# Kernel tuning notes

Hardware: AMD Instinct MI355X
Metric: run time of the kernel (lower is better)

The kernel has to match this reference:

```python
import jax, jax.numpy as jnp
import numpy as np
from jax import lax

H = 1024
L = 9


def setup_inputs() -> dict:
    key = jax.random.key(0)
    ks = jax.random.split(key, 10)
    B, T = 64, 512
    hidden_states = jax.random.normal(ks[0], (B, T, H), dtype=jnp.float32)
    attention_mask = jnp.ones((B, T), dtype=jnp.int32)
    labels = jax.random.randint(ks[1], (B, T), 0, L).astype(jnp.int64)
    W1 = 0.02 * jax.random.normal(ks[2], (H, H // 2), dtype=jnp.float32)
    b1 = jnp.zeros((H // 2,), dtype=jnp.float32)
    W2 = 0.02 * jax.random.normal(ks[3], (H // 2, L), dtype=jnp.float32)
    b2 = jnp.zeros((L,), dtype=jnp.float32)
    start_transitions = 0.1 * jax.random.normal(ks[4], (L,), dtype=jnp.float32)
    end_transitions = 0.1 * jax.random.normal(ks[5], (L,), dtype=jnp.float32)
    transitions = 0.1 * jax.random.normal(ks[6], (L, L), dtype=jnp.float32)
    return {"hidden_states": hidden_states, "attention_mask": attention_mask,
            "labels": labels, "W1": W1, "b1": b1, "W2": W2, "b2": b2,
            "start_transitions": start_transitions,
            "end_transitions": end_transitions, "transitions": transitions}


def crf_nll(logits, tags, mask, start_t, end_t, trans):
    """torchcrf negative mean log-likelihood. logits [B,T,L], tags [B,T], mask [B,T] bool."""
    emis = jnp.swapaxes(logits, 0, 1)          # [T,B,L]
    tg = jnp.swapaxes(tags, 0, 1)              # [T,B]
    m = jnp.swapaxes(mask, 0, 1).astype(logits.dtype)  # [T,B]

    # --- numerator: score of the gold path ---
    e0 = jnp.take_along_axis(emis[0], tg[0][:, None], axis=1)[:, 0]
    score0 = start_t[tg[0]] + e0

    def num_step(carry, inp):
        score, prev = carry
        e, t, mi = inp
        step = trans[prev, t] + jnp.take_along_axis(e, t[:, None], axis=1)[:, 0]
        score = score + step * mi
        prev = jnp.where(mi > 0, t, prev)
        return (score, prev), None

    (num, last_tag), _ = lax.scan(num_step, (score0, tg[0]), (emis[1:], tg[1:], m[1:]))
    num = num + end_t[last_tag]

    # --- denominator: forward algorithm (log partition) ---
    alpha0 = start_t[None, :] + emis[0]        # [B,L]

    def den_step(alpha, inp):
        e, mi = inp
        nxt = jax.nn.logsumexp(alpha[:, :, None] + trans[None, :, :] + e[:, None, :], axis=1)
        return jnp.where(mi[:, None] > 0, nxt, alpha), None

    alpha, _ = lax.scan(den_step, alpha0, (emis[1:], m[1:]))
    den = jax.nn.logsumexp(alpha + end_t[None, :], axis=1)

    return -jnp.mean(num - den)


def reference(hidden_states, attention_mask, labels, W1, b1, W2, b2,
              start_transitions, end_transitions, transitions):
    # dropout is identity in eval mode
    x = jax.nn.relu(hidden_states @ W1 + b1)
    logits = x @ W2 + b2                        # [B,T,L]

    valid = labels != -100
    crf_labels = jnp.where(valid, labels, 0)
    mask = (attention_mask.astype(bool)) & valid
    mask = mask.at[:, 0].set(True)              # first timestep always on

    loss = crf_nll(logits, crf_labels, mask,
                   start_transitions, end_transitions, transitions)
    return logits, loss
```

## Files before the change

kernel.cpp:

```cpp
#include <hip/hip_runtime.h>
#include <hip/hip_bf16.h>

#define B_  64
#define T_  512
#define H_  1024
#define HC  512
#define L9  9

typedef short short8 __attribute__((ext_vector_type(8)));
typedef float f32x16 __attribute__((ext_vector_type(16)));

__device__ __forceinline__ unsigned short f2bf(float x) {
  unsigned u = __float_as_uint(x);
  u += 0x7FFFu + ((u >> 16) & 1u);
  return (unsigned short)(u >> 16);
}
__device__ __forceinline__ float bf2f(unsigned short h) {
  return __uint_as_float(((unsigned)h) << 16);
}

__device__ __forceinline__ void gload_lds16(const void* g, void* l) {
  __builtin_amdgcn_global_load_lds((const __attribute__((address_space(1))) unsigned*)g,
                                   (__attribute__((address_space(3))) unsigned*)l, 16, 0, 0);
}

__global__ void conv_w1(const float* __restrict__ w1, unsigned short* __restrict__ w1b) {
  int idx = blockIdx.x * 256 + threadIdx.x;
  int n = idx & 511, kq = idx >> 9;
  float x0 = w1[(kq * 4 + 0) * HC + n];
  float x1 = w1[(kq * 4 + 1) * HC + n];
  float x2 = w1[(kq * 4 + 2) * HC + n];
  float x3 = w1[(kq * 4 + 3) * HC + n];
  uint2 d;
  d.x = (unsigned)f2bf(x0) | ((unsigned)f2bf(x1) << 16);
  d.y = (unsigned)f2bf(x2) | ((unsigned)f2bf(x3) << 16);
  *(uint2*)(w1b + n * 1024 + kq * 4) = d;
}

__global__ __launch_bounds__(256, 2) void gemm1(
    const float* __restrict__ hs, const unsigned short* __restrict__ w1b,
    const float* __restrict__ b1, const float* __restrict__ w2,
    const float* __restrict__ b2, float* __restrict__ logits, float* __restrict__ wsE)
{
  __shared__ __align__(16) unsigned char smem[80128];
  unsigned short* ldsA = (unsigned short*)smem;
  unsigned short* ldsB = (unsigned short*)(smem + 8192);

  const int tid  = threadIdx.x;
  const int lane = tid & 63;
  const int w    = tid >> 6;
  const int row0 = blockIdx.x * 64;

  f32x16 acc[2][4];
  #pragma unroll
  for (int m = 0; m < 2; ++m)
    #pragma unroll
    for (int n = 0; n < 4; ++n)
      #pragma unroll
      for (int e = 0; e < 16; ++e) acc[m][n][e] = 0.f;

  const int arow = tid >> 2;
  const int aj4  = tid & 3;
  const float* aSrc = hs + (size_t)(row0 + arow) * H_ + aj4 * 16;
  unsigned short* aDst0 = ldsA + arow * 64 + (((aj4 * 2 + 0) ^ (arow & 7)) * 8);
  unsigned short* aDst1 = ldsA + arow * 64 + (((aj4 * 2 + 1) ^ (arow & 7)) * 8);

  const int bn   = lane >> 3;
  const int bjsw = ((lane & 7) ^ bn) * 8;

  for (int kt = 0; kt < 16; ++kt) {
    const int k0 = kt * 64;
    float4 v0 = *(const float4*)(aSrc + k0);
    float4 v1 = *(const float4*)(aSrc + k0 + 4);
    float4 v2 = *(const float4*)(aSrc + k0 + 8);
    float4 v3 = *(const float4*)(aSrc + k0 + 12);
    uint4 p0, p1;
    p0.x = (unsigned)f2bf(v0.x) | ((unsigned)f2bf(v0.y) << 16);
    p0.y = (unsigned)f2bf(v0.z) | ((unsigned)f2bf(v0.w) << 16);
    p0.z = (unsigned)f2bf(v1.x) | ((unsigned)f2bf(v1.y) << 16);
    p0.w = (unsigned)f2bf(v1.z) | ((unsigned)f2bf(v1.w) << 16);
    p1.x = (unsigned)f2bf(v2.x) | ((unsigned)f2bf(v2.y) << 16);
    p1.y = (unsigned)f2bf(v2.z) | ((unsigned)f2bf(v2.w) << 16);
    p1.z = (unsigned)f2bf(v3.x) | ((unsigned)f2bf(v3.y) << 16);
    p1.w = (unsigned)f2bf(v3.z) | ((unsigned)f2bf(v3.w) << 16);
    *(uint4*)aDst0 = p0;
    *(uint4*)aDst1 = p1;
    #pragma unroll
    for (int i = 0; i < 16; ++i) {
      int cc = w * 16 + i;
      gload_lds16(w1b + (size_t)(cc * 8 + bn) * 1024 + k0 + bjsw,
                  (unsigned char*)ldsB + cc * 1024);
    }
    __syncthreads();
    #pragma unroll
    for (int ks = 0; ks < 4; ++ks) {
      const int blk = (((ks * 2 + (lane >> 5)) ^ (lane & 7)) * 8);
      short8 aF[2], bF[4];
      #pragma unroll
      for (int m = 0; m < 2; ++m)
        aF[m] = *(const short8*)(ldsA + (m * 32 + (lane & 31)) * 64 + blk);
      #pragma unroll
      for (int n = 0; n < 4; ++n)
        bF[n] = *(const short8*)(ldsB + (w * 128 + n * 32 + (lane & 31)) * 64 + blk);
      #pragma unroll
      for (int m = 0; m < 2; ++m)
        #pragma unroll
        for (int n = 0; n < 4; ++n)
          acc[m][n] = __builtin_amdgcn_mfma_f32_32x32x16_bf16(aF[m], bF[n], acc[m][n], 0, 0, 0);
    }
    __syncthreads();
  }

  float b1v[4];
  #pragma unroll
  for (int n = 0; n < 4; ++n) b1v[n] = b1[w * 128 + n * 32 + (lane & 31)];

  #pragma unroll
  for (int m = 0; m < 2; ++m)
    #pragma unroll
    for (int n = 0; n < 4; ++n) {
      int col = w * 128 + n * 32 + (lane & 31);
      int csw = col & 7;
      unsigned char* cbase = smem + col * 128 + (lane >> 5) * 8;
      #pragma unroll
      for (int q = 0; q < 4; ++q) {
        unsigned short h0 = f2bf(fmaxf(acc[m][n][q * 4 + 0] + b1v[n], 0.f));
        unsigned short h1 = f2bf(fmaxf(acc[m][n][q * 4 + 1] + b1v[n], 0.f));
        unsigned short h2 = f2bf(fmaxf(acc[m][n][q * 4 + 2] + b1v[n], 0.f));
        unsigned short h3 = f2bf(fmaxf(acc[m][n][q * 4 + 3] + b1v[n], 0.f));
        uint2 d;
        d.x = (unsigned)h0 | ((unsigned)h1 << 16);
        d.y = (unsigned)h2 | ((unsigned)h3 << 16);
        *(uint2*)(cbase + (((4 * m + q) ^ csw) * 16)) = d;
      }
    }

  unsigned short* ldsW2 = (unsigned short*)(smem + 65536);
  float* sAcc = (float*)(smem + 77824);
  {
    int c0 = tid * 2;
    #pragma unroll
    for (int cc = c0; cc < c0 + 2; ++cc)
      #pragma unroll
      for (int l = 0; l < 9; ++l) ldsW2[cc * 12 + l] = f2bf(w2[cc * 9 + l]);
    for (int i = tid; i < 576; i += 256) sAcc[i] = 0.f;
  }
  __syncthreads();

  {
    int r = tid & 63, ch = tid >> 6;
    int rblk = r >> 3, rlow = r & 7;
    float s[9];
    #pragma unroll
    for (int l = 0; l < 9; ++l) s[l] = 0.f;
    for (int c = ch * 128; c < ch * 128 + 128; ++c) {
      float xv = bf2f(*(const unsigned short*)(smem + c * 128 + ((rblk ^ (c & 7)) * 16) + rlow * 2));
      uint2 wa = *(const uint2*)(ldsW2 + c * 12);
      uint2 wb = *(const uint2*)(ldsW2 + c * 12 + 4);
      unsigned wcv = *(const unsigned*)(ldsW2 + c * 12 + 8);
      s[0] = fmaf(xv, __uint_as_float(wa.x << 16), s[0]);
      s[1] = fmaf(xv, __uint_as_float(wa.x & 0xFFFF0000u), s[1]);
      s[2] = fmaf(xv, __uint_as_float(wa.y << 16), s[2]);
      s[3] = fmaf(xv, __uint_as_float(wa.y & 0xFFFF0000u), s[3]);
      s[4] = fmaf(xv, __uint_as_float(wb.x << 16), s[4]);
      s[5] = fmaf(xv, __uint_as_float(wb.x & 0xFFFF0000u), s[5]);
      s[6] = fmaf(xv, __uint_as_float(wb.y << 16), s[6]);
      s[7] = fmaf(xv, __uint_as_float(wb.y & 0xFFFF0000u), s[7]);
      s[8] = fmaf(xv, __uint_as_float(wcv << 16), s[8]);
    }
    #pragma unroll
    for (int l = 0; l < 9; ++l) atomicAdd(&sAcc[r * 9 + l], s[l]);
  }
  __syncthreads();

  {
    int bb = row0 >> 9, t0g = row0 & 511;
    for (int v = tid; v < 576; v += 256) {
      int r = v / 9, l = v - r * 9;
      float val = sAcc[v] + b2[l];
      logits[(size_t)(row0 + r) * 9 + l] = val;
      wsE[(size_t)((t0g + r) * 9 + l) * 64 + bb] = __expf(val);
    }
  }
}

#define NCH 64
#define CHL 8
__global__ __launch_bounds__(64, 1) void crf_chunks(
    const float* __restrict__ wsE, const int* __restrict__ labels,
    const int* __restrict__ amask, const float* __restrict__ logits,
    const float* __restrict__ trans, float* __restrict__ wsG)
{
  __shared__ float sT[81];
  int b = threadIdx.x;
  for (int i = b; i < 81; i += 64) sT[i] = trans[i];
  __syncthreads();
  int c = blockIdx.x;

  float eT[81];
  #pragma unroll
  for (int i = 0; i < 81; ++i) eT[i] = __expf(sT[i]);

  float G[81];
  #pragma unroll
  for (int i = 0; i < 9; ++i)
    #pragma unroll
    for (int j = 0; j < 9; ++j) G[i * 9 + j] = (i == j) ? 1.f : 0.f;

  float logC = 0.f, sumN = 0.f;
  int ft = -1, lt = -1, prevL = -1;

  int tstart = (c == 0) ? 1 : c * CHL;
  int tend = c * CHL + CHL;

  for (int t = tstart; t < tend; ++t) {
    int lab = labels[b * T_ + t];
    int am  = amask[b * T_ + t];
    bool valid = (lab != -100);
    int tag = valid ? lab : 0;
    bool m = (am != 0) && valid;

    float E[9];
    #pragma unroll
    for (int j = 0; j < 9; ++j) E[j] = wsE[(size_t)(t * 9 + j) * 64 + b];

    float emis = logits[(size_t)b * (T_ * 9) + t * 9 + tag];
    int pidx = (prevL < 0 ? 0 : prevL) * 9 + tag;
    float trTerm = (prevL >= 0) ? sT[pidx] : 0.f;
    sumN += m ? (emis + trTerm) : 0.f;
    ft = (m && ft < 0) ? tag : ft;
    lt = m ? tag : lt;
    prevL = m ? tag : prevL;

    #pragma unroll
    for (int i = 0; i < 9; ++i) {
      float nG[9];
      #pragma unroll
      for (int j = 0; j < 9; ++j) {
        float s = G[i * 9 + 0] * eT[j];
        #pragma unroll
        for (int k = 1; k < 9; ++k) s = fmaf(G[i * 9 + k], eT[k * 9 + j], s);
        nG[j] = s * E[j];
      }
      #pragma unroll
      for (int j = 0; j < 9; ++j) G[i * 9 + j] = m ? nG[j] : G[i * 9 + j];
    }
    float mx = G[0];
    #pragma unroll
    for (int e = 1; e < 81; ++e) mx = fmaxf(mx, G[e]);
    float rv = 1.0f / mx;
    logC += __logf(mx);
    #pragma unroll
    for (int e = 0; e < 81; ++e) G[e] *= rv;
  }

  float* o = wsG + (size_t)c * 88 * 64 + b;
  #pragma unroll
  for (int e = 0; e < 81; ++e) o[e * 64] = G[e];
  o[81 * 64] = logC;
  o[82 * 64] = sumN;
  o[83 * 64] = __int_as_float(ft);
  o[84 * 64] = __int_as_float(lt);
}

__global__ __launch_bounds__(64, 1) void crf_combine(
    const float* __restrict__ wsE, const int* __restrict__ labels,
    const float* __restrict__ logits,
    const float* __restrict__ start_t, const float* __restrict__ end_t,
    const float* __restrict__ trans, const float* __restrict__ wsG,
    float* __restrict__ out_loss)
{
  __shared__ float sT[81];
  int b = threadIdx.x;
  for (int i = b; i < 81; i += 64) sT[i] = trans[i];
  __syncthreads();

  int lab0 = labels[b * T_];
  int tag0 = (lab0 != -100) ? lab0 : 0;
  float num = start_t[tag0] + logits[(size_t)b * (T_ * 9) + tag0];
  int prev = tag0;

  float P[9];
  #pragma unroll
  for (int j = 0; j < 9; ++j) P[j] = __expf(start_t[j]) * wsE[j * 64 + b];
  float mx = P[0];
  #pragma unroll
  for (int j = 1; j < 9; ++j) mx = fmaxf(mx, P[j]);
  float C = __logf(mx);
  float rv = 1.0f / mx;
  #pragma unroll
  for (int j = 0; j < 9; ++j) P[j] *= rv;

  for (int c = 0; c < NCH; ++c) {
    const float* g = wsG + (size_t)c * 88 * 64 + b;
    float Gm[81];
    #pragma unroll
    for (int e = 0; e < 81; ++e) Gm[e] = g[e * 64];
    float logC = g[81 * 64];
    float sumN = g[82 * 64];
    int ft = __float_as_int(g[83 * 64]);
    int lt = __float_as_int(g[84 * 64]);

    float nP[9];
    #pragma unroll
    for (int j = 0; j < 9; ++j) {
      float s = P[0] * Gm[j];
      #pragma unroll
      for (int i = 1; i < 9; ++i) s = fmaf(P[i], Gm[i * 9 + j], s);
      nP[j] = s;
    }
    float mxs = nP[0];
    #pragma unroll
    for (int j = 1; j < 9; ++j) mxs = fmaxf(mxs, nP[j]);
    float rvs = 1.0f / mxs;
    C += logC + __logf(mxs);
    #pragma unroll
    for (int j = 0; j < 9; ++j) P[j] = nP[j] * rvs;

    if (ft >= 0) {
      num += sumN + sT[prev * 9 + ft];
      prev = lt;
    }
  }

  float sfin = 0.f;
  #pragma unroll
  for (int j = 0; j < 9; ++j) sfin = fmaf(P[j], __expf(end_t[j]), sfin);
  float den = C + __logf(sfin);
  num += end_t[prev];
  float d = num - den;
  #pragma unroll
  for (int off = 32; off > 0; off >>= 1) d += __shfl_down(d, off);
  if (b == 0) out_loss[0] = -d * (1.0f / 64.0f);
}

extern "C" void kernel_launch(void* const* d_in, const int* in_sizes, int n_in,
                              void* d_out, int out_size, void* d_ws, size_t ws_size,
                              hipStream_t stream) {
  (void)in_sizes; (void)n_in; (void)out_size; (void)ws_size;
  const float* hs     = (const float*)d_in[0];
  const int*   am     = (const int*)  d_in[1];
  const int*   labels = (const int*)  d_in[2];
  const float* w1     = (const float*)d_in[3];
  const float* b1     = (const float*)d_in[4];
  const float* w2     = (const float*)d_in[5];
  const float* b2     = (const float*)d_in[6];
  const float* st     = (const float*)d_in[7];
  const float* en     = (const float*)d_in[8];
  const float* tr     = (const float*)d_in[9];
  float* out = (float*)d_out;

  unsigned short* wsBn = (unsigned short*)d_ws;
  float*          wsE  = (float*)((char*)d_ws + 1048576);
  float*          wsG  = (float*)((char*)d_ws + 1048576 + 1179648);

  conv_w1    <<<512, 256, 0, stream>>>(w1, wsBn);
  gemm1      <<<512, 256, 0, stream>>>(hs, wsBn, b1, w2, b2, out, wsE);
  crf_chunks <<<64,  64,  0, stream>>>(wsE, labels, am, out, tr, wsG);
  crf_combine<<<1,   64,  0, stream>>>(wsE, labels, out, st, en, tr, wsG, out + 294912);
}
```

Baseline: 336.6 us.

## Double-buffer GEMM K-loop, repack W1 layout, use hardware bf16 pack, tree-fold CRF chunks

The GEMM main loop now uses two LDS buffers with a 32-wide K step: loads for the next tile are issued before computing the current one, and a partial vmcnt wait replaces the full barrier pair. The aim is to overlap global-to-LDS traffic with MFMA work. W1 is converted into a new K-group-major bf16 layout with 16-byte writes, and bf16 conversion uses v_cvt_pk_bf16_f32 instead of software rounding. The serial CRF combine over 64 chunks is split into an 8-block fold kernel plus a final kernel over 8 partial products, which shortens the serial chain at the cost of an extra launch.

```diff
diff --git a/kernel.cpp b/kernel.cpp
--- a/kernel.cpp
+++ b/kernel.cpp
@@ -1,11 +1,8 @@
 #include <hip/hip_runtime.h>
-#include <hip/hip_bf16.h>
-
-#define B_  64
+
 #define T_  512
 #define H_  1024
 #define HC  512
-#define L9  9
 
 typedef short short8 __attribute__((ext_vector_type(8)));
 typedef float f32x16 __attribute__((ext_vector_type(16)));
@@ -18,7 +15,11 @@
 __device__ __forceinline__ float bf2f(unsigned short h) {
   return __uint_as_float(((unsigned)h) << 16);
 }
-
+__device__ __forceinline__ unsigned cvtpk(float lo, float hi) {
+  unsigned r;
+  asm("v_cvt_pk_bf16_f32 %0, %1, %2" : "=v"(r) : "v"(lo), "v"(hi));
+  return r;
+}
 __device__ __forceinline__ void gload_lds16(const void* g, void* l) {
   __builtin_amdgcn_global_load_lds((const __attribute__((address_space(1))) unsigned*)g,
                                    (__attribute__((address_space(3))) unsigned*)l, 16, 0, 0);
@@ -26,15 +27,17 @@
 
 __global__ void conv_w1(const float* __restrict__ w1, unsigned short* __restrict__ w1b) {
   int idx = blockIdx.x * 256 + threadIdx.x;
-  int n = idx & 511, kq = idx >> 9;
-  float x0 = w1[(kq * 4 + 0) * HC + n];
-  float x1 = w1[(kq * 4 + 1) * HC + n];
-  float x2 = w1[(kq * 4 + 2) * HC + n];
-  float x3 = w1[(kq * 4 + 3) * HC + n];
-  uint2 d;
-  d.x = (unsigned)f2bf(x0) | ((unsigned)f2bf(x1) << 16);
-  d.y = (unsigned)f2bf(x2) | ((unsigned)f2bf(x3) << 16);
-  *(uint2*)(w1b + n * 1024 + kq * 4) = d;
+  int n = idx & 511, o = idx >> 9;
+  const float* src = w1 + (size_t)(o * 8) * HC + n;
+  float v[8];
+  #pragma unroll
+  for (int j = 0; j < 8; ++j) v[j] = src[j * HC];
+  uint4 d;
+  d.x = cvtpk(v[0], v[1]);
+  d.y = cvtpk(v[2], v[3]);
+  d.z = cvtpk(v[4], v[5]);
+  d.w = cvtpk(v[6], v[7]);
+  *(uint4*)(w1b + (size_t)idx * 8) = d;
 }
 
 __global__ __launch_bounds__(256, 2) void gemm1(
@@ -43,9 +46,6 @@
     const float* __restrict__ b2, float* __restrict__ logits, float* __restrict__ wsE)
 {
   __shared__ __align__(16) unsigned char smem[80128];
-  unsigned short* ldsA = (unsigned short*)smem;
-  unsigned short* ldsB = (unsigned short*)(smem + 8192);
-
   const int tid  = threadIdx.x;
   const int lane = tid & 63;
   const int w    = tid >> 6;
@@ -59,57 +59,104 @@
       #pragma unroll
       for (int e = 0; e < 16; ++e) acc[m][n][e] = 0.f;
 
-  const int arow = tid >> 2;
-  const int aj4  = tid & 3;
-  const float* aSrc = hs + (size_t)(row0 + arow) * H_ + aj4 * 16;
-  unsigned short* aDst0 = ldsA + arow * 64 + (((aj4 * 2 + 0) ^ (arow & 7)) * 8);
-  unsigned short* aDst1 = ldsA + arow * 64 + (((aj4 * 2 + 1) ^ (arow & 7)) * 8);
-
-  const int bn   = lane >> 3;
-  const int bjsw = ((lane & 7) ^ bn) * 8;
-
-  for (int kt = 0; kt < 16; ++kt) {
-    const int k0 = kt * 64;
-    float4 v0 = *(const float4*)(aSrc + k0);
-    float4 v1 = *(const float4*)(aSrc + k0 + 4);
-    float4 v2 = *(const float4*)(aSrc + k0 + 8);
-    float4 v3 = *(const float4*)(aSrc + k0 + 12);
-    uint4 p0, p1;
-    p0.x = (unsigned)f2bf(v0.x) | ((unsigned)f2bf(v0.y) << 16);
-    p0.y = (unsigned)f2bf(v0.z) | ((unsigned)f2bf(v0.w) << 16);
-    p0.z = (unsigned)f2bf(v1.x) | ((unsigned)f2bf(v1.y) << 16);
-    p0.w = (unsigned)f2bf(v1.z) | ((unsigned)f2bf(v1.w) << 16);
-    p1.x = (unsigned)f2bf(v2.x) | ((unsigned)f2bf(v2.y) << 16);
-    p1.y = (unsigned)f2bf(v2.z) | ((unsigned)f2bf(v2.w) << 16);
-    p1.z = (unsigned)f2bf(v3.x) | ((unsigned)f2bf(v3.y) << 16);
-    p1.w = (unsigned)f2bf(v3.z) | ((unsigned)f2bf(v3.w) << 16);
-    *(uint4*)aDst0 = p0;
-    *(uint4*)aDst1 = p1;
-    #pragma unroll
-    for (int i = 0; i < 16; ++i) {
-      int cc = w * 16 + i;
-      gload_lds16(w1b + (size_t)(cc * 8 + bn) * 1024 + k0 + bjsw,
-                  (unsigned char*)ldsB + cc * 1024);
-    }
-    __syncthreads();
-    #pragma unroll
-    for (int ks = 0; ks < 4; ++ks) {
-      const int blk = (((ks * 2 + (lane >> 5)) ^ (lane & 7)) * 8);
+  const int ar  = tid >> 2;
+  const int akg = tid & 3;
+  const float* aSrc = hs + (size_t)(row0 + ar) * H_ + akg * 8;
+  const int aoff = ar * 64 + ((akg ^ ((ar >> 1) & 3)) * 16);
+
+  {
+    float4 av0 = *(const float4*)(aSrc);
+    float4 av1 = *(const float4*)(aSrc + 4);
+    unsigned char* bbase = smem + 4096;
+    #pragma unroll
+    for (int i = 0; i < 8; ++i) {
+      int kg = i >> 1;
+      int c0 = ((i & 1) * 4 + w) * 64;
+      gload_lds16(w1b + ((size_t)kg * 512 + c0 + lane) * 8, bbase + (kg * 512 + c0) * 16);
+    }
+    uint4 ap;
+    ap.x = cvtpk(av0.x, av0.y); ap.y = cvtpk(av0.z, av0.w);
+    ap.z = cvtpk(av1.x, av1.y); ap.w = cvtpk(av1.z, av1.w);
+    *(uint4*)(smem + aoff) = ap;
+  }
+
+  for (int kt = 0; kt < 31; ++kt) {
+    const int cur = kt & 1, nxt = cur ^ 1;
+    float4 av0 = *(const float4*)(aSrc + (kt + 1) * 32);
+    float4 av1 = *(const float4*)(aSrc + (kt + 1) * 32 + 4);
+    {
+      unsigned char* bbase = smem + nxt * 36864 + 4096;
+      int o0 = (kt + 1) * 4;
+      #pragma unroll
+      for (int i = 0; i < 8; ++i) {
+        int kg = i >> 1;
+        int c0 = ((i & 1) * 4 + w) * 64;
+        gload_lds16(w1b + ((size_t)(o0 + kg) * 512 + c0 + lane) * 8,
+                    bbase + (kg * 512 + c0) * 16);
+      }
+    }
+    asm volatile("s_waitcnt vmcnt(10) lgkmcnt(0)" ::: "memory");
+    __builtin_amdgcn_s_barrier();
+    __builtin_amdgcn_sched_barrier(0);
+    {
+      const unsigned char* abase = smem + cur * 36864;
+      const unsigned char* bbase = abase + 4096;
+      #pragma unroll
+      for (int ks = 0; ks < 2; ++ks) {
+        const int kg = ks * 2 + (lane >> 5);
+        short8 aF[2], bF[4];
+        #pragma unroll
+        for (int m = 0; m < 2; ++m) {
+          int r = m * 32 + (lane & 31);
+          aF[m] = *(const short8*)(abase + r * 64 + ((kg ^ ((r >> 1) & 3)) * 16));
+        }
+        #pragma unroll
+        for (int n = 0; n < 4; ++n) {
+          int c = w * 128 + n * 32 + (lane & 31);
+          bF[n] = *(const short8*)(bbase + (kg * 512 + c) * 16);
+        }
+        #pragma unroll
+        for (int m = 0; m < 2; ++m)
+          #pragma unroll
+          for (int n = 0; n < 4; ++n)
+            acc[m][n] = __builtin_amdgcn_mfma_f32_32x32x16_bf16(aF[m], bF[n], acc[m][n], 0, 0, 0);
+      }
+    }
+    {
+      uint4 ap;
+      ap.x = cvtpk(av0.x, av0.y); ap.y = cvtpk(av0.z, av0.w);
+      ap.z = cvtpk(av1.x, av1.y); ap.w = cvtpk(av1.z, av1.w);
+      *(uint4*)(smem + nxt * 36864 + aoff) = ap;
+    }
+  }
+  asm volatile("s_waitcnt vmcnt(0) lgkmcnt(0)" ::: "memory");
+  __builtin_amdgcn_s_barrier();
+  __builtin_amdgcn_sched_barrier(0);
+  {
+    const unsigned char* abase = smem + 36864;
+    const unsigned char* bbase = abase + 4096;
+    #pragma unroll
+    for (int ks = 0; ks < 2; ++ks) {
+      const int kg = ks * 2 + (lane >> 5);
       short8 aF[2], bF[4];
       #pragma unroll
-      for (int m = 0; m < 2; ++m)
-        aF[m] = *(const short8*)(ldsA + (m * 32 + (lane & 31)) * 64 + blk);
-      #pragma unroll
-      for (int n = 0; n < 4; ++n)
-        bF[n] = *(const short8*)(ldsB + (w * 128 + n * 32 + (lane & 31)) * 64 + blk);
+      for (int m = 0; m < 2; ++m) {
+        int r = m * 32 + (lane & 31);
+        aF[m] = *(const short8*)(abase + r * 64 + ((kg ^ ((r >> 1) & 3)) * 16));
+      }
+      #pragma unroll
+      for (int n = 0; n < 4; ++n) {
+        int c = w * 128 + n * 32 + (lane & 31);
+        bF[n] = *(const short8*)(bbase + (kg * 512 + c) * 16);
+      }
       #pragma unroll
       for (int m = 0; m < 2; ++m)
         #pragma unroll
         for (int n = 0; n < 4; ++n)
           acc[m][n] = __builtin_amdgcn_mfma_f32_32x32x16_bf16(aF[m], bF[n], acc[m][n], 0, 0, 0);
     }
-    __syncthreads();
-  }
+  }
+  __syncthreads();
 
   float b1v[4];
   #pragma unroll
@@ -124,13 +171,13 @@
       unsigned char* cbase = smem + col * 128 + (lane >> 5) * 8;
       #pragma unroll
       for (int q = 0; q < 4; ++q) {
-        unsigned short h0 = f2bf(fmaxf(acc[m][n][q * 4 + 0] + b1v[n], 0.f));
-        unsigned short h1 = f2bf(fmaxf(acc[m][n][q * 4 + 1] + b1v[n], 0.f));
-        unsigned short h2 = f2bf(fmaxf(acc[m][n][q * 4 + 2] + b1v[n], 0.f));
-        unsigned short h3 = f2bf(fmaxf(acc[m][n][q * 4 + 3] + b1v[n], 0.f));
+        float v0 = fmaxf(acc[m][n][q * 4 + 0] + b1v[n], 0.f);
+        float v1 = fmaxf(acc[m][n][q * 4 + 1] + b1v[n], 0.f);
+        float v2 = fmaxf(acc[m][n][q * 4 + 2] + b1v[n], 0.f);
+        float v3 = fmaxf(acc[m][n][q * 4 + 3] + b1v[n], 0.f);
         uint2 d;
-        d.x = (unsigned)h0 | ((unsigned)h1 << 16);
-        d.y = (unsigned)h2 | ((unsigned)h3 << 16);
+        d.x = cvtpk(v0, v1);
+        d.y = cvtpk(v2, v3);
         *(uint2*)(cbase + (((4 * m + q) ^ csw) * 16)) = d;
       }
     }
@@ -263,11 +310,75 @@
   o[84 * 64] = __int_as_float(lt);
 }
 
-__global__ __launch_bounds__(64, 1) void crf_combine(
+__global__ __launch_bounds__(64, 1) void crf_fold(
+    const float* __restrict__ wsG, const float* __restrict__ trans,
+    float* __restrict__ wsG2)
+{
+  __shared__ float sT[81];
+  int b = threadIdx.x;
+  for (int i = b; i < 81; i += 64) sT[i] = trans[i];
+  __syncthreads();
+  int f = blockIdx.x;
+
+  float G[81];
+  #pragma unroll
+  for (int i = 0; i < 9; ++i)
+    #pragma unroll
+    for (int j = 0; j < 9; ++j) G[i * 9 + j] = (i == j) ? 1.f : 0.f;
+  float logC = 0.f, sumN = 0.f;
+  int ft = -1, lt = -1;
+
+  for (int cc = 0; cc < 8; ++cc) {
+    const float* g = wsG + (size_t)(f * 8 + cc) * 88 * 64 + b;
+    float Gm[81];
+    #pragma unroll
+    for (int e = 0; e < 81; ++e) Gm[e] = g[e * 64];
+    float lC = g[81 * 64], sN = g[82 * 64];
+    int fte = __float_as_int(g[83 * 64]);
+    int lte = __float_as_int(g[84 * 64]);
+
+    #pragma unroll
+    for (int i = 0; i < 9; ++i) {
+      float row[9];
+      #pragma unroll
+      for (int j = 0; j < 9; ++j) {
+        float s = G[i * 9 + 0] * Gm[j];
+        #pragma unroll
+        for (int k = 1; k < 9; ++k) s = fmaf(G[i * 9 + k], Gm[k * 9 + j], s);
+        row[j] = s;
+      }
+      #pragma unroll
+      for (int j = 0; j < 9; ++j) G[i * 9 + j] = row[j];
+    }
+    float mx = G[0];
+    #pragma unroll
+    for (int e = 1; e < 81; ++e) mx = fmaxf(mx, G[e]);
+    logC += lC + __logf(mx);
+    float rv = 1.0f / mx;
+    #pragma unroll
+    for (int e = 0; e < 81; ++e) G[e] *= rv;
+
+    if (fte >= 0) {
+      sumN += sN + (lt >= 0 ? sT[lt * 9 + fte] : 0.f);
+      if (ft < 0) ft = fte;
+      lt = lte;
+    }
+  }
+
+  float* o = wsG2 + (size_t)f * 88 * 64 + b;
+  #pragma unroll
+  for (int e = 0; e < 81; ++e) o[e * 64] = G[e];
+  o[81 * 64] = logC;
+  o[82 * 64] = sumN;
+  o[83 * 64] = __int_as_float(ft);
+  o[84 * 64] = __int_as_float(lt);
+}
+
+__global__ __launch_bounds__(64, 1) void crf_final(
     const float* __restrict__ wsE, const int* __restrict__ labels,
     const float* __restrict__ logits,
     const float* __restrict__ start_t, const float* __restrict__ end_t,
-    const float* __restrict__ trans, const float* __restrict__ wsG,
+    const float* __restrict__ trans, const float* __restrict__ wsG2,
     float* __restrict__ out_loss)
 {
   __shared__ float sT[81];
@@ -291,8 +402,8 @@
   #pragma unroll
   for (int j = 0; j < 9; ++j) P[j] *= rv;
 
-  for (int c = 0; c < NCH; ++c) {
-    const float* g = wsG + (size_t)c * 88 * 64 + b;
+  for (int c = 0; c < 8; ++c) {
+    const float* g = wsG2 + (size_t)c * 88 * 64 + b;
     float Gm[81];
     #pragma unroll
     for (int e = 0; e < 81; ++e) Gm[e] = g[e * 64];
@@ -352,10 +463,12 @@
 
   unsigned short* wsBn = (unsigned short*)d_ws;
   float*          wsE  = (float*)((char*)d_ws + 1048576);
-  float*          wsG  = (float*)((char*)d_ws + 1048576 + 1179648);
-
-  conv_w1    <<<512, 256, 0, stream>>>(w1, wsBn);
-  gemm1      <<<512, 256, 0, stream>>>(hs, wsBn, b1, w2, b2, out, wsE);
-  crf_chunks <<<64,  64,  0, stream>>>(wsE, labels, am, out, tr, wsG);
-  crf_combine<<<1,   64,  0, stream>>>(wsE, labels, out, st, en, tr, wsG, out + 294912);
-}
+  float*          wsG  = (float*)((char*)d_ws + 2228224);
+  float*          wsG2 = (float*)((char*)d_ws + 3670016);
+
+  conv_w1   <<<256, 256, 0, stream>>>(w1, wsBn);
+  gemm1     <<<512, 256, 0, stream>>>(hs, wsBn, b1, w2, b2, out, wsE);
+  crf_chunks<<<64,  64,  0, stream>>>(wsE, labels, am, out, tr, wsG);
+  crf_fold  <<<8,   64,  0, stream>>>(wsG, tr, wsG2);
+  crf_final <<<1,   64,  0, stream>>>(wsE, labels, out, st, en, tr, wsG2, out + 294912);
+}
```

Result: faster. 299.2 us (-11.1%).
